# Optimization experiments

Measured on AMD Instinct MI355X. Metric: run time of the kernel, lower is better.

Reference implementation:

```python
import jax, jax.numpy as jnp
import numpy as np

B, G, P, H = 32, 5000, 5000, 64
N = B * G
E_CO, E_GG = 1600000, 100000

def _bn(x, g, b):
    # BatchNorm1d in training mode: biased batch stats, eps=1e-5
    m = x.mean(0); v = x.var(0)
    return g * (x - m) * jax.lax.rsqrt(v + 1e-5) + b

def _renorm(t):
    # nn.Embedding(max_norm=True) -> rows renormed to L2 norm <= 1
    n = jnp.linalg.norm(t, axis=1, keepdims=True)
    return t * jnp.minimum(1.0, 1.0 / jnp.maximum(n, 1e-12))

def _sgconv(x, src, dst, w, W, b):
    # SGConv(K=1): gcn_norm (self-loops w=1, symmetric deg norm) spmm, then Linear
    n = x.shape[0]
    sl = jnp.arange(n)
    s = jnp.concatenate([src, sl]); d = jnp.concatenate([dst, sl])
    ww = jnp.concatenate([w, jnp.ones((n,), x.dtype)])
    deg = jax.ops.segment_sum(ww, d, num_segments=n)
    dinv = jnp.where(deg > 0, jax.lax.rsqrt(deg), 0.0)
    coef = dinv[s] * ww * dinv[d]
    agg = jax.ops.segment_sum(coef[:, None] * x[s], d, num_segments=n)
    return agg @ W.T + b

def _mlp3(x, W, b, g, bt):
    # MLP([h,h,h]): Lin-BN-ReLU-Lin-BN (trailing ReLU stripped by [:-1])
    h = jax.nn.relu(_bn(x @ W[0].T + b[0], g[0], bt[0]))
    return _bn(h @ W[1].T + b[1], g[1], bt[1])

def _gears(x, pert_idx, ei_co, w_co, ei_go, w_go, ei_bg, w_bg,
           gene_tab, pos_tab, go_tab, bg_tab, bn_g, bn_b, sg_W, sg_b,
           mlp_W, mlp_b, mlp_g, mlp_bt,
           rec_W1, rec_b1, rec_g1, rec_bt1, rec_W2, rec_b2, rec_g2, rec_bt2,
           indv_w1, indv_b1,
           cg_W1, cg_b1, cg_g1, cg_bt1, cg_W2, cg_b2, cg_g2, cg_bt2,
           indv_w2, indv_b2):
    nb = pert_idx.shape[0]
    ng = gene_tab.shape[0]
    emb = jnp.tile(_renorm(gene_tab), (nb, 1))                     # [B*G,H]
    base = jax.nn.relu(_bn(emb, bn_g[0], bn_b[0]))                 # bn_emb + emb_trans
    pos = jnp.tile(_renorm(pos_tab), (nb, 1))
    pos = _sgconv(pos, ei_co[0], ei_co[1], w_co, sg_W[0], sg_b[0]) # 1 gene-pos GNN layer, no trailing relu
    base = base + 0.2 * pos
    base = _mlp3(base, mlp_W[1], mlp_b[1], mlp_g[1], mlp_bt[1])    # emb_trans_v2
    pgo = _sgconv(_renorm(go_tab), ei_go[0], ei_go[1], w_go, sg_W[1], sg_b[1])
    pbg = _sgconv(_renorm(bg_tab), ei_bg[0], ei_bg[1], w_bg, sg_W[2], sg_b[2])
    pglob = _mlp3(pgo + pbg, mlp_W[0], mlp_b[0], mlp_g[0], mlp_bt[0])  # pert_emb_comb_trans
    base = base.reshape(nb, ng, -1)
    # one valid pert per graph -> pert_track reduces to a gather; pert_fuse then broadcast-add
    emb_total = _mlp3(pglob[pert_idx], mlp_W[2], mlp_b[2], mlp_g[2], mlp_bt[2])  # [B,H]
    base = base + emb_total[:, None, :]
    base = base.reshape(nb * ng, -1)
    base = jax.nn.relu(_bn(base, bn_g[1], bn_b[1]))                # bn_pert_base + transform
    h = jax.nn.relu(_bn(base @ rec_W1.T + rec_b1, rec_g1, rec_bt1))
    out = _bn(h @ rec_W2.T + rec_b2, rec_g2, rec_bt2).reshape(nb, ng, -1)
    w1 = jnp.einsum('bgh,gh->bg', out, indv_w1) + indv_b1          # per-gene decoder 1
    cg = jax.nn.relu(_bn(w1 @ cg_W1.T + cg_b1, cg_g1, cg_bt1))
    cg = _bn(cg @ cg_W2.T + cg_b2, cg_g2, cg_bt2)                  # cross_gene_state [B,H]
    cat = jnp.concatenate([w1[..., None], jnp.broadcast_to(cg[:, None, :], (nb, ng, cg.shape[-1]))], -1)
    out2 = jnp.einsum('bgk,gk->bg', cat, indv_w2) + indv_b2        # per-gene decoder 2
    return out2 + x.reshape(nb, ng)

def setup_inputs():
    ks = jax.random.split(jax.random.key(0), 48)
    rn = lambda i, sh, s=0.05: jax.random.normal(ks[i], sh, jnp.float32) * s
    return {
        "x": rn(0, (N,), 1.0),
        "pert_idx": jax.random.randint(ks[1], (B,), 0, P),
        "ei_co": jax.random.randint(ks[2], (2, E_CO), 0, N),
        "w_co": jax.random.uniform(ks[3], (E_CO,), jnp.float32),
        "ei_go": jax.random.randint(ks[4], (2, E_GG), 0, P),
        "w_go": jax.random.uniform(ks[5], (E_GG,), jnp.float32),
        "ei_bg": jax.random.randint(ks[6], (2, E_GG), 0, P),
        "w_bg": jax.random.uniform(ks[7], (E_GG,), jnp.float32),
        "gene_tab": rn(8, (G, H), 1.0),
        "pos_tab": rn(9, (G, H), 1.0),
        "go_tab": rn(10, (P, H), 1.0),
        "bg_tab": rn(11, (P, H), 1.0),
        "bn_g": jnp.ones((2, H)), "bn_b": jnp.zeros((2, H)),
        "sg_W": rn(12, (3, H, H)), "sg_b": jnp.zeros((3, H)),
        "mlp_W": rn(13, (3, 2, H, H)), "mlp_b": jnp.zeros((3, 2, H)),
        "mlp_g": jnp.ones((3, 2, H)), "mlp_bt": jnp.zeros((3, 2, H)),
        "rec_W1": rn(14, (2 * H, H)), "rec_b1": jnp.zeros((2 * H,)),
        "rec_g1": jnp.ones((2 * H,)), "rec_bt1": jnp.zeros((2 * H,)),
        "rec_W2": rn(15, (H, 2 * H)), "rec_b2": jnp.zeros((H,)),
        "rec_g2": jnp.ones((H,)), "rec_bt2": jnp.zeros((H,)),
        "indv_w1": rn(16, (G, H)), "indv_b1": rn(17, (G,)),
        "cg_W1": rn(18, (H, G), 0.01), "cg_b1": jnp.zeros((H,)),
        "cg_g1": jnp.ones((H,)), "cg_bt1": jnp.zeros((H,)),
        "cg_W2": rn(19, (H, H)), "cg_b2": jnp.zeros((H,)),
        "cg_g2": jnp.ones((H,)), "cg_bt2": jnp.zeros((H,)),
        "indv_w2": rn(20, (G, H + 1)), "indv_b2": rn(21, (G,)),
    }

def reference(x, pert_idx, ei_co, w_co, ei_go, w_go, ei_bg, w_bg,
              gene_tab, pos_tab, go_tab, bg_tab, bn_g, bn_b, sg_W, sg_b,
              mlp_W, mlp_b, mlp_g, mlp_bt,
              rec_W1, rec_b1, rec_g1, rec_bt1, rec_W2, rec_b2, rec_g2, rec_bt2,
              indv_w1, indv_b1,
              cg_W1, cg_b1, cg_g1, cg_bt1, cg_W2, cg_b2, cg_g2, cg_bt2,
              indv_w2, indv_b2):
    return _gears(x, pert_idx, ei_co, w_co, ei_go, w_go, ei_bg, w_bg,
                  gene_tab, pos_tab, go_tab, bg_tab, bn_g, bn_b, sg_W, sg_b,
                  mlp_W, mlp_b, mlp_g, mlp_bt,
                  rec_W1, rec_b1, rec_g1, rec_bt1, rec_W2, rec_b2, rec_g2, rec_bt2,
                  indv_w1, indv_b1,
                  cg_W1, cg_b1, cg_g1, cg_bt1, cg_W2, cg_b2, cg_g2, cg_bt2,
                  indv_w2, indv_b2)
```

## Files before the change

kernel.cpp:

```cpp
#include <hip/hip_runtime.h>

typedef unsigned int u32;
typedef unsigned short u16;

constexpr int Gn  = 5000;
constexpr int Bn  = 32;
constexpr int Pn  = 5000;
constexpr int Nn  = Bn * Gn;
constexpr int ECO = 1600000;
constexpr int EGG = 100000;
constexpr int NTILES = Nn / 128;
constexpr int PTILES = 40;

constexpr int oS1 = 0, oS2 = 128, oS3 = 256, oS4 = 384, oS5 = 640, oSG = 768, oSP1 = 896, oSP2 = 1024;
constexpr int oZERO = 1536;
constexpr int oA1 = 2048, oB1 = 2112, oA2 = 2176, oB2 = 2240;
constexpr int oA4 = 2304, oB4 = 2432;
constexpr int oA5 = 2560, oB5 = 2624;
constexpr int oAG = 2688, oBG = 2752;
constexpr int oAP1 = 2816, oBP1 = 2880, oAP2 = 2944, oBP2 = 3008;
constexpr int oAvec = 3072, oCvec = 3136, oCcP = 3200;
constexpr int oM  = 4096, oM1 = 8192;
constexpr int oE2 = 16384, oEMB = 18432, oCGRAW = 20480, oCG2 = 22528;
constexpr int oRG  = 24576;
constexpr int oRP  = oRG  + Gn * 64;
constexpr int oQ   = oRP  + Gn * 64;
constexpr int oRGO = oQ   + Gn * 64;
constexpr int oRBG = oRGO + Pn * 64;
constexpr int oAGO = oRBG + Pn * 64;
constexpr int oABG = oAGO + Pn * 64;
constexpr int oM1B = oABG + Pn * 64;
constexpr int oM2B = oM1B + Pn * 64;
constexpr int oDGO = oM2B + Pn * 64;
constexpr int oDBG = oDGO + Pn;
constexpr int oDEG = oDBG + Pn;
constexpr int oW1  = oDEG + Nn;
constexpr int oBUF0 = oW1 + Nn;
constexpr int oBUF1 = oBUF0 + Nn * 64;
constexpr size_t WS_FLOATS = (size_t)oBUF1 + (size_t)Nn * 64;

__device__ inline u16 f2bf(float f) {
  u32 u = __float_as_uint(f);
  u = (u + 0x7fffu + ((u >> 16) & 1u)) >> 16;
  return (u16)u;
}
__device__ inline float bflo(u32 v) { return __uint_as_float(v << 16); }
__device__ inline float bfhi(u32 v) { return __uint_as_float(v & 0xffff0000u); }
__device__ inline float bf2f(u16 v) { return __uint_as_float((u32)v << 16); }

typedef __attribute__((ext_vector_type(8))) short short8v;
typedef __attribute__((ext_vector_type(4))) float f32x4;

__global__ __launch_bounds__(256) void kzero(float* p, int n) {
  int i = blockIdx.x * 256 + threadIdx.x;
  if (i < n) p[i] = 0.f;
}

__global__ __launch_bounds__(256) void krenorm(const float* __restrict__ in, float* __restrict__ out,
                                               float* __restrict__ stats, u16* __restrict__ outb, int rows) {
  int lane = threadIdx.x & 63, wv = threadIdx.x >> 6;
  int gw = blockIdx.x * 4 + wv, nw = gridDim.x * 4;
  float ps = 0.f, pq = 0.f;
  for (int r = gw; r < rows; r += nw) {
    float v = in[r * 64 + lane];
    float sq = v * v;
    for (int off = 32; off; off >>= 1) sq += __shfl_xor(sq, off, 64);
    float nn = sqrtf(sq);
    float s = fminf(1.f, 1.f / fmaxf(nn, 1e-12f));
    float o = v * s;
    out[r * 64 + lane] = o;
    if (outb) outb[r * 64 + lane] = f2bf(o);
    ps += o; pq += o * o;
  }
  if (!stats) return;
  __shared__ float red[4][64], red2[4][64];
  red[wv][lane] = ps; red2[wv][lane] = pq;
  __syncthreads();
  if (wv == 0) {
    float s = red[0][lane] + red[1][lane] + red[2][lane] + red[3][lane];
    float q = red2[0][lane] + red2[1][lane] + red2[2][lane] + red2[3][lane];
    atomicAdd(&stats[lane], s);
    atomicAdd(&stats[64 + lane], q);
  }
}

__global__ void kfin(const float* __restrict__ stats, const float* __restrict__ g,
                     const float* __restrict__ bt, float* __restrict__ a, float* __restrict__ b,
                     int cols, float invn) {
  int c = blockIdx.x * 64 + threadIdx.x;
  if (c >= cols) return;
  float mean = stats[c] * invn;
  float var = stats[cols + c] * invn - mean * mean;
  float sc = g[c] * rsqrtf(var + 1e-5f);
  a[c] = sc;
  b[c] = bt[c] - mean * sc;
}

__global__ __launch_bounds__(256) void ksmallmat(const float* __restrict__ A, const float* __restrict__ Bm,
                                                 float alpha, const float* __restrict__ bias,
                                                 const float* __restrict__ bv1, const float* __restrict__ bv2,
                                                 float beta, float* __restrict__ Mout, int mpitch,
                                                 float* __restrict__ cvec) {
  __shared__ float As[4096], Bs[4096];
  int t = threadIdx.x;
  for (int m = 0; m < 16; m++) { As[m * 256 + t] = A[m * 256 + t]; Bs[m * 256 + t] = Bm[m * 256 + t]; }
  __syncthreads();
  int j = t & 63, ig = t >> 6;
  for (int ii = 0; ii < 16; ii++) {
    int i = ig * 16 + ii;
    float acc = 0.f;
    for (int k = 0; k < 64; k++) acc += As[i * 64 + k] * Bs[k * 64 + j];
    Mout[i * mpitch + j] = alpha * acc;
  }
  if (cvec && t < 64) {
    float acc = bias ? bias[t] : 0.f;
    for (int k = 0; k < 64; k++) {
      float bb = (bv1 ? bv1[k] : 0.f) + (bv2 ? bv2[k] : 0.f);
      acc += beta * As[t * 64 + k] * bb;
    }
    cvec[t] = acc;
  }
}

__global__ __launch_bounds__(256) void khist(const int* __restrict__ dst, int* __restrict__ cnt,
                                             int* __restrict__ ticket, int E) {
  int e = blockIdx.x * 256 + threadIdx.x;
  if (e < E) ticket[e] = atomicAdd(&cnt[dst[e]], 1);
}

__global__ __launch_bounds__(256) void kscan1(const int* __restrict__ cnt, int* __restrict__ bsum, int n) {
  __shared__ int sh[256];
  int b = blockIdx.x, t = threadIdx.x;
  int base = b * 1024 + t * 4;
  int s = 0;
#pragma unroll
  for (int j = 0; j < 4; j++) { int i = base + j; if (i < n) s += cnt[i]; }
  sh[t] = s; __syncthreads();
  for (int d = 128; d; d >>= 1) { if (t < d) sh[t] += sh[t + d]; __syncthreads(); }
  if (t == 0) bsum[b] = sh[0];
}
__global__ __launch_bounds__(256) void kscan2(int* bsum, int nb, int* off_n) {
  __shared__ int sh[256];
  int t = threadIdx.x;
  int v = (t < nb) ? bsum[t] : 0;
  sh[t] = v;
  __syncthreads();
  for (int d = 1; d < 256; d <<= 1) {
    int u = (t >= d) ? sh[t - d] : 0;
    __syncthreads();
    sh[t] += u;
    __syncthreads();
  }
  if (t < nb) bsum[t] = sh[t] - v;
  if (t == nb - 1 && off_n) *off_n = sh[t];
}
__global__ __launch_bounds__(256) void kscan3(int* __restrict__ cnt, const int* __restrict__ bsum, int n) {
  __shared__ int sh[256];
  int b = blockIdx.x, t = threadIdx.x;
  int base = b * 1024 + t * 4;
  int c0 = (base + 0 < n) ? cnt[base + 0] : 0;
  int c1 = (base + 1 < n) ? cnt[base + 1] : 0;
  int c2 = (base + 2 < n) ? cnt[base + 2] : 0;
  int c3 = (base + 3 < n) ? cnt[base + 3] : 0;
  int tot = c0 + c1 + c2 + c3;
  sh[t] = tot; __syncthreads();
  for (int d = 1; d < 256; d <<= 1) {
    int v = (t >= d) ? sh[t - d] : 0;
    __syncthreads();
    sh[t] += v;
    __syncthreads();
  }
  int excl = sh[t] - tot + bsum[b];
  if (base + 0 < n) cnt[base + 0] = excl;
  if (base + 1 < n) cnt[base + 1] = excl + c0;
  if (base + 2 < n) cnt[base + 2] = excl + c0 + c1;
  if (base + 3 < n) cnt[base + 3] = excl + c0 + c1 + c2;
}

__global__ __launch_bounds__(256) void kfillt(const int* __restrict__ src, const int* __restrict__ dst,
                                              const float* __restrict__ w, const int* __restrict__ off,
                                              const int* __restrict__ ticket, float2* __restrict__ pack, int E) {
  int e = blockIdx.x * 256 + threadIdx.x;
  if (e >= E) return;
  int d = dst[e];
  int pos = off[d] + ticket[e];
  pack[pos] = make_float2(w[e], __int_as_float(src[e]));
}

__global__ __launch_bounds__(256) void kdinvrow(const int* __restrict__ off, const float2* __restrict__ pack,
                                                float* __restrict__ dinv, int n) {
  int i = blockIdx.x * 256 + threadIdx.x;
  if (i >= n) return;
  int b0 = off[i], b1 = off[i + 1];
  float s = 1.f;
  for (int j = b0; j < b1; j++) s += pack[j].x;
  dinv[i] = rsqrtf(s);
}

__global__ __launch_bounds__(256) void kgather(const int* __restrict__ off, const float2* __restrict__ pack,
                                               const float* __restrict__ dinv, const float* __restrict__ tab,
                                               u16* __restrict__ aggb, int pitch, int coff, int n) {
  int lane = threadIdx.x & 63;
  int wv = blockIdx.x * 4 + (threadIdx.x >> 6);
  int nw = gridDim.x * 4;
  for (int i = wv; i < n; i += nw) {
    int b0 = off[i], b1 = off[i + 1];
    float di = dinv[i];
    float acc = di * tab[(i % Gn) * 64 + lane];
    for (int base = b0; base < b1; base += 64) {
      int m = b1 - base; if (m > 64) m = 64;
      float cj = 0.f; int idxj = 0;
      if (lane < m) {
        float2 p = pack[base + lane];
        int s = __float_as_int(p.y);
        cj = p.x * dinv[s];
        idxj = (s % Gn) * 64;
      }
      int j = 0;
      for (; j + 1 < m; j += 2) {
        float c0 = __shfl(cj, j, 64);     int i0 = __shfl(idxj, j, 64);
        float c1 = __shfl(cj, j + 1, 64); int i1 = __shfl(idxj, j + 1, 64);
        float t0 = tab[i0 + lane];
        float t1 = tab[i1 + lane];
        acc = fmaf(c0, t0, acc);
        acc = fmaf(c1, t1, acc);
      }
      if (j < m) {
        float c0 = __shfl(cj, j, 64); int i0 = __shfl(idxj, j, 64);
        acc = fmaf(c0, tab[i0 + lane], acc);
      }
    }
    acc *= di;
    aggb[(size_t)i * pitch + coff + lane] = f2bf(acc);
  }
}

template <int K, int OUTC, bool PRE, bool EB, bool PERG, bool STATS, bool OUTF32, bool STATB>
__global__ __launch_bounds__(256, 3) void mfgemm(
    const u16* __restrict__ Xb, const float* __restrict__ Wg, const float* __restrict__ bias,
    const float* __restrict__ pa, const float* __restrict__ pb,
    const float* __restrict__ perg, u16* __restrict__ Ybf, float* __restrict__ stats,
    float* __restrict__ statB, int rows) {
  constexpr int NT  = OUTC / 16;
  constexpr int KH  = K / 32;
  constexpr int SLK = K / 8;
  constexpr int SLO = OUTC / 8;
  constexpr int XROW = (K > OUTC ? K : OUTC) * 2;
  __shared__ __align__(16) unsigned char xsb[128 * XROW];
  __shared__ __align__(16) unsigned char wsb[OUTC * K * 2];
  __shared__ float sstat[STATS ? 2 * OUTC : 1];
  __shared__ float sstatB[STATB ? 128 : 1];
  int t = threadIdx.x;
  int l = t & 63, w = t >> 6, lrow = l & 15, lk = l >> 4;
  int R0 = blockIdx.x * 128;

  for (int idx = t; idx < OUTC * SLK; idx += 256) {
    int oc = idx / SLK, s8 = idx % SLK;
    const float* wp = &Wg[oc * K + s8 * 8];
    uint4 o;
    o.x = (u32)f2bf(wp[0]) | ((u32)f2bf(wp[1]) << 16);
    o.y = (u32)f2bf(wp[2]) | ((u32)f2bf(wp[3]) << 16);
    o.z = (u32)f2bf(wp[4]) | ((u32)f2bf(wp[5]) << 16);
    o.w = (u32)f2bf(wp[6]) | ((u32)f2bf(wp[7]) << 16);
    *(uint4*)&wsb[oc * (2 * K) + ((s8 * 16) ^ ((oc & 7) << 4))] = o;
  }
  if constexpr (STATS) for (int idx = t; idx < 2 * OUTC; idx += 256) sstat[idx] = 0.f;
  if constexpr (STATB) for (int idx = t; idx < 128; idx += 256) sstatB[idx] = 0.f;

#pragma unroll
  for (int m = 0; m < SLK / 2; m++) {
    int f = m * 256 + t;
    int r = f / SLK, s8 = f % SLK;
    uint4 u = *(const uint4*)&Xb[(size_t)(R0 + r) * K + s8 * 8];
    if constexpr (PRE) {
      int c0 = s8 * 8;
      float4 A0 = *(const float4*)&pa[c0];
      float4 A1 = *(const float4*)&pa[c0 + 4];
      const float* pbb = EB ? &pb[((R0 + r) / Gn) * 64] : pb;
      float4 B0 = *(const float4*)&pbb[c0];
      float4 B1 = *(const float4*)&pbb[c0 + 4];
      float v0 = fmaxf(fmaf(A0.x, bflo(u.x), B0.x), 0.f);
      float v1 = fmaxf(fmaf(A0.y, bfhi(u.x), B0.y), 0.f);
      float v2 = fmaxf(fmaf(A0.z, bflo(u.y), B0.z), 0.f);
      float v3 = fmaxf(fmaf(A0.w, bfhi(u.y), B0.w), 0.f);
      float v4 = fmaxf(fmaf(A1.x, bflo(u.z), B1.x), 0.f);
      float v5 = fmaxf(fmaf(A1.y, bfhi(u.z), B1.y), 0.f);
      float v6 = fmaxf(fmaf(A1.z, bflo(u.w), B1.z), 0.f);
      float v7 = fmaxf(fmaf(A1.w, bfhi(u.w), B1.w), 0.f);
      u.x = (u32)f2bf(v0) | ((u32)f2bf(v1) << 16);
      u.y = (u32)f2bf(v2) | ((u32)f2bf(v3) << 16);
      u.z = (u32)f2bf(v4) | ((u32)f2bf(v5) << 16);
      u.w = (u32)f2bf(v6) | ((u32)f2bf(v7) << 16);
    }
    *(uint4*)&xsb[r * XROW + ((s8 * 16) ^ ((r & 7) << 4))] = u;
  }
  float bcol[NT];
#pragma unroll
  for (int nt = 0; nt < NT; nt++) bcol[nt] = bias[nt * 16 + lrow];
  __syncthreads();

  short8v af[2][KH];
#pragma unroll
  for (int rt = 0; rt < 2; rt++)
#pragma unroll
    for (int h = 0; h < KH; h++) {
      int row = w * 32 + rt * 16 + lrow;
      af[rt][h] = *(const short8v*)&xsb[row * XROW + ((h * 64 + lk * 16) ^ ((row & 7) << 4))];
    }
  f32x4 acc[2][NT];
#pragma unroll
  for (int rt = 0; rt < 2; rt++)
#pragma unroll
    for (int nt = 0; nt < NT; nt++) {
      f32x4 z = {0.f, 0.f, 0.f, 0.f};
      acc[rt][nt] = z;
    }
#pragma unroll
  for (int nt = 0; nt < NT; nt++) {
    int brow = nt * 16 + lrow;
#pragma unroll
    for (int h = 0; h < KH; h++) {
      short8v bfr = *(const short8v*)&wsb[brow * (2 * K) + ((h * 64 + lk * 16) ^ ((brow & 7) << 4))];
      acc[0][nt] = __builtin_amdgcn_mfma_f32_16x16x32_bf16(af[0][h], bfr, acc[0][nt], 0, 0, 0);
      acc[1][nt] = __builtin_amdgcn_mfma_f32_16x16x32_bf16(af[1][h], bfr, acc[1][nt], 0, 0, 0);
    }
  }
  __syncthreads();

  float sS[NT], sQ[NT], sB0[NT], sB1[NT];
#pragma unroll
  for (int nt = 0; nt < NT; nt++) { sS[nt] = 0.f; sQ[nt] = 0.f; sB0[nt] = 0.f; sB1[nt] = 0.f; }
  int hiStart = STATB ? (R0 / Gn + 1) * Gn : 0x7fffffff;
  float* Yf = (float*)Ybf;
#pragma unroll
  for (int rt = 0; rt < 2; rt++) {
#pragma unroll
    for (int r = 0; r < 4; r++) {
      int orow = w * 32 + rt * 16 + lk * 4 + r;
      int grow = R0 + orow;
      bool valid = grow < rows;
      int qoff = 0;
      if constexpr (PERG) qoff = (grow % Gn) * 64;
#pragma unroll
      for (int nt = 0; nt < NT; nt++) {
        float v = acc[rt][nt][r] + bcol[nt];
        if constexpr (PERG) v += perg[qoff + nt * 16 + lrow];
        if (valid) {
          if constexpr (STATS) { sS[nt] += v; sQ[nt] += v * v; }
          if constexpr (STATB) { if (grow >= hiStart) sB1[nt] += v; else sB0[nt] += v; }
        }
        if constexpr (OUTF32) {
          if (valid) Yf[(size_t)grow * OUTC + nt * 16 + lrow] = v;
        } else {
          *(u16*)&xsb[orow * (2 * OUTC) + ((2 * (nt * 16 + lrow)) ^ ((orow & 7) << 4))] = f2bf(v);
        }
      }
    }
  }
  if constexpr (STATS) {
#pragma unroll
    for (int nt = 0; nt < NT; nt++) {
      atomicAdd(&sstat[nt * 16 + lrow], sS[nt]);
      atomicAdd(&sstat[OUTC + nt * 16 + lrow], sQ[nt]);
    }
  }
  if constexpr (STATB) {
#pragma unroll
    for (int nt = 0; nt < NT; nt++) {
      atomicAdd(&sstatB[nt * 16 + lrow], sB0[nt]);
      atomicAdd(&sstatB[64 + nt * 16 + lrow], sB1[nt]);
    }
  }
  __syncthreads();

  if constexpr (!OUTF32) {
#pragma unroll
    for (int m = 0; m < SLO / 2; m++) {
      int f = m * 256 + t;
      int r = f / SLO, c8 = f % SLO;
      uint4 o = *(const uint4*)&xsb[r * (2 * OUTC) + ((16 * c8) ^ ((r & 7) << 4))];
      *(uint4*)&Ybf[(size_t)(R0 + r) * OUTC + c8 * 8] = o;
    }
  }
  if constexpr (STATS)
    for (int idx = t; idx < 2 * OUTC; idx += 256) atomicAdd(&stats[idx], sstat[idx]);
  if constexpr (STATB) {
    int bLo = R0 / Gn;
    for (int idx = t; idx < 128; idx += 256) {
      int b = bLo + (idx >> 6);
      if (b < Bn) atomicAdd(&statB[b * 64 + (idx & 63)], sstatB[idx]);
    }
  }
}

__global__ __launch_bounds__(256) void kfinS3e2(const float* __restrict__ S2, const float* __restrict__ g,
                                                const float* __restrict__ bt, const float* __restrict__ a2,
                                                const float* __restrict__ b2, const float* __restrict__ emb,
                                                const float* __restrict__ S3B,
                                                float* __restrict__ Avec, float* __restrict__ e2) {
  __shared__ float a3s[64], b3s[64];
  int t = threadIdx.x;
  if (t < 64) {
    float a2c = a2[t], b2c = b2[t];
    float su = 0.f, sxc = 0.f, sc2 = 0.f;
    for (int b = 0; b < Bn; b++) {
      float cb = b2c + emb[b * 64 + t];
      float sb = S3B[b * 64 + t];
      su += cb;
      sxc += cb * sb;
      sc2 += cb * cb;
    }
    float Su = a2c * S2[t] + (float)Gn * su;
    float Sq = a2c * a2c * S2[64 + t] + 2.f * a2c * sxc + (float)Gn * sc2;
    float mean = Su * (1.f / Nn);
    float var = Sq * (1.f / Nn) - mean * mean;
    float sc = g[t] * rsqrtf(var + 1e-5f);
    float sh = bt[t] - mean * sc;
    a3s[t] = sc; b3s[t] = sh;
    Avec[t] = sc * a2c;
  }
  __syncthreads();
  for (int idx = t; idx < 2048; idx += 256) {
    int c = idx & 63;
    e2[idx] = a3s[c] * (b2[c] + emb[idx]) + b3s[c];
  }
}

__global__ __launch_bounds__(256) void k13_kernel(const u16* __restrict__ R2, const float* __restrict__ a5,
                                                  const float* __restrict__ b5, const float* __restrict__ iw1,
                                                  const float* __restrict__ ib1, float* __restrict__ w1out,
                                                  int rows) {
  int t = blockIdx.x * 256 + threadIdx.x;
  int i = t >> 4, j = t & 15;
  if (i >= rows) return;
  int g = i % Gn;
  uint2 u = *(const uint2*)&R2[(size_t)i * 64 + j * 4];
  float rx = bflo(u.x), ry = bfhi(u.x), rz = bflo(u.y), rw = bfhi(u.y);
  float4 a = ((const float4*)a5)[j];
  float4 b = ((const float4*)b5)[j];
  float4 w = ((const float4*)iw1)[g * 16 + j];
  float p = (a.x * rx + b.x) * w.x + (a.y * ry + b.y) * w.y +
            (a.z * rz + b.z) * w.z + (a.w * rw + b.w) * w.w;
  for (int off = 8; off; off >>= 1) p += __shfl_xor(p, off, 64);
  if (j == 0) w1out[i] = p + ib1[g];
}

__global__ __launch_bounds__(256) void kinitcg(const float* __restrict__ cgb1, float* __restrict__ cgraw) {
  int idx = blockIdx.x * 256 + threadIdx.x;
  if (idx < Bn * 64) cgraw[idx] = cgb1[idx & 63];
}

__global__ __launch_bounds__(256) void kcg1s(const float* __restrict__ w1, const float* __restrict__ cgW1,
                                             float* __restrict__ cgraw) {
  __shared__ float w1s[64 * 36];
  __shared__ float cgs[64 * 65];
  int t = threadIdx.x;
  int k0 = blockIdx.x * 64;
  int kmax = Gn - k0; if (kmax > 64) kmax = 64;
  for (int idx = t; idx < 2048; idx += 256) {
    int row = idx >> 6, k = idx & 63;
    w1s[k * 36 + row] = (k < kmax) ? w1[row * Gn + k0 + k] : 0.f;
  }
  for (int idx = t; idx < 4096; idx += 256) {
    int col = idx >> 6, k = idx & 63;
    cgs[k * 65 + col] = (k < kmax) ? cgW1[col * Gn + k0 + k] : 0.f;
  }
  __syncthreads();
  int col = t & 63, rg = t >> 6;
  float acc[8];
#pragma unroll
  for (int i = 0; i < 8; i++) acc[i] = 0.f;
  for (int k = 0; k < 64; k++) {
    float wk = cgs[k * 65 + col];
    const float* wr = &w1s[k * 36 + rg * 8];
    float4 r0 = *(const float4*)wr;
    float4 r1 = *(const float4*)(wr + 4);
    acc[0] = fmaf(r0.x, wk, acc[0]);
    acc[1] = fmaf(r0.y, wk, acc[1]);
    acc[2] = fmaf(r0.z, wk, acc[2]);
    acc[3] = fmaf(r0.w, wk, acc[3]);
    acc[4] = fmaf(r1.x, wk, acc[4]);
    acc[5] = fmaf(r1.y, wk, acc[5]);
    acc[6] = fmaf(r1.z, wk, acc[6]);
    acc[7] = fmaf(r1.w, wk, acc[7]);
  }
#pragma unroll
  for (int i = 0; i < 8; i++) atomicAdd(&cgraw[(rg * 8 + i) * 64 + col], acc[i]);
}

__global__ __launch_bounds__(256) void kcg2(const float* __restrict__ cgraw, const float* __restrict__ g1,
                                            const float* __restrict__ bt1, const float* __restrict__ W2,
                                            const float* __restrict__ b2, const float* __restrict__ g2,
                                            const float* __restrict__ bt2, float* __restrict__ cg2out) {
  int t = threadIdx.x, c = t & 63, bg = t >> 6;
  __shared__ float hmid[2048], sred[4][64], qred[4][64], asc[64], bsh[64];
  float y[8];
  float ps = 0.f, pq = 0.f;
  for (int jb = 0; jb < 8; jb++) {
    int b = bg * 8 + jb;
    float v = cgraw[b * 64 + c];
    y[jb] = v; ps += v; pq += v * v;
  }
  sred[bg][c] = ps; qred[bg][c] = pq;
  __syncthreads();
  if (t < 64) {
    float s = sred[0][t] + sred[1][t] + sred[2][t] + sred[3][t];
    float q = qred[0][t] + qred[1][t] + qred[2][t] + qred[3][t];
    float mean = s * (1.f / 32.f), var = q * (1.f / 32.f) - mean * mean;
    float sc = g1[t] * rsqrtf(var + 1e-5f);
    asc[t] = sc; bsh[t] = bt1[t] - mean * sc;
  }
  __syncthreads();
  for (int jb = 0; jb < 8; jb++) { int b = bg * 8 + jb; hmid[b * 64 + c] = fmaxf(asc[c] * y[jb] + bsh[c], 0.f); }
  __syncthreads();
  ps = 0.f; pq = 0.f;
  for (int jb = 0; jb < 8; jb++) {
    int b = bg * 8 + jb;
    float a = b2[c];
    for (int k = 0; k < 64; k++) a += hmid[b * 64 + k] * W2[c * 64 + k];
    y[jb] = a; ps += a; pq += a * a;
  }
  sred[bg][c] = ps; qred[bg][c] = pq;
  __syncthreads();
  if (t < 64) {
    float s = sred[0][t] + sred[1][t] + sred[2][t] + sred[3][t];
    float q = qred[0][t] + qred[1][t] + qred[2][t] + qred[3][t];
    float mean = s * (1.f / 32.f), var = q * (1.f / 32.f) - mean * mean;
    float sc = g2[t] * rsqrtf(var + 1e-5f);
    asc[t] = sc; bsh[t] = bt2[t] - mean * sc;
  }
  __syncthreads();
  for (int jb = 0; jb < 8; jb++) { int b = bg * 8 + jb; cg2out[b * 64 + c] = asc[c] * y[jb] + bsh[c]; }
}

__global__ __launch_bounds__(256) void kemb(const u16* __restrict__ m2, const float* __restrict__ aP2,
                                            const float* __restrict__ bP2, const int* __restrict__ pidx,
                                            const float* __restrict__ Wm, const float* __restrict__ bv,
                                            const float* __restrict__ gg, const float* __restrict__ btv,
                                            float* __restrict__ emb) {
  int t = threadIdx.x, c = t & 63, bg = t >> 6;
  __shared__ float xin[2048], hmid[2048], sred[4][64], qred[4][64], asc[64], bsh[64];
  for (int idx = t; idx < 2048; idx += 256) {
    int b = idx >> 6, cc = idx & 63;
    xin[idx] = aP2[cc] * bf2f(m2[(size_t)pidx[b] * 64 + cc]) + bP2[cc];
  }
  __syncthreads();
  float y[8];
  float ps = 0.f, pq = 0.f;
  for (int jb = 0; jb < 8; jb++) {
    int b = bg * 8 + jb;
    float a = bv[c];
    for (int k = 0; k < 64; k++) a += xin[b * 64 + k] * Wm[c * 64 + k];
    y[jb] = a; ps += a; pq += a * a;
  }
  sred[bg][c] = ps; qred[bg][c] = pq;
  __syncthreads();
  if (t < 64) {
    float s = sred[0][t] + sred[1][t] + sred[2][t] + sred[3][t];
    float q = qred[0][t] + qred[1][t] + qred[2][t] + qred[3][t];
    float mean = s * (1.f / 32.f), var = q * (1.f / 32.f) - mean * mean;
    float sc = gg[t] * rsqrtf(var + 1e-5f);
    asc[t] = sc; bsh[t] = btv[t] - mean * sc;
  }
  __syncthreads();
  for (int jb = 0; jb < 8; jb++) { int b = bg * 8 + jb; hmid[b * 64 + c] = fmaxf(asc[c] * y[jb] + bsh[c], 0.f); }
  __syncthreads();
  ps = 0.f; pq = 0.f;
  for (int jb = 0; jb < 8; jb++) {
    int b = bg * 8 + jb;
    float a = bv[64 + c];
    for (int k = 0; k < 64; k++) a += hmid[b * 64 + k] * Wm[4096 + c * 64 + k];
    y[jb] = a; ps += a; pq += a * a;
  }
  sred[bg][c] = ps; qred[bg][c] = pq;
  __syncthreads();
  if (t < 64) {
    float s = sred[0][t] + sred[1][t] + sred[2][t] + sred[3][t];
    float q = qred[0][t] + qred[1][t] + qred[2][t] + qred[3][t];
    float mean = s * (1.f / 32.f), var = q * (1.f / 32.f) - mean * mean;
    float sc = gg[64 + t] * rsqrtf(var + 1e-5f);
    asc[t] = sc; bsh[t] = btv[64 + t] - mean * sc;
  }
  __syncthreads();
  for (int jb = 0; jb < 8; jb++) { int b = bg * 8 + jb; emb[b * 64 + c] = asc[c] * y[jb] + bsh[c]; }
}

__global__ __launch_bounds__(256) void kfinal(const float* __restrict__ w1, const float* __restrict__ cg2,
                                              const float* __restrict__ iw2, const float* __restrict__ ib2,
                                              const float* __restrict__ x, float* __restrict__ out) {
  __shared__ float iws[64 * 65], cgs[2048];
  int t = threadIdx.x;
  int g0 = blockIdx.x * 64;
  for (int idx = t; idx < 64 * 65; idx += 256) {
    int gi = g0 * 65 + idx;
    iws[idx] = (gi < Gn * 65) ? iw2[gi] : 0.f;
  }
  for (int idx = t; idx < 2048; idx += 256) cgs[idx] = cg2[idx];
  __syncthreads();
  int gl = t & 63, bg = t >> 6;
  int g = g0 + gl;
  if (g >= Gn) return;
  float bias = ib2[g];
  for (int jb = 0; jb < 8; jb++) {
    int b = bg * 8 + jb;
    float acc = w1[b * Gn + g] * iws[gl * 65] + bias;
    for (int k = 0; k < 64; k++) acc += cgs[b * 64 + k] * iws[gl * 65 + 1 + k];
    out[b * Gn + g] = acc + x[b * Gn + g];
  }
}

extern "C" void kernel_launch(void* const* d_in, const int* in_sizes, int n_in,
                              void* d_out, int out_size, void* d_ws, size_t ws_size,
                              hipStream_t stream) {
  (void)in_sizes; (void)n_in; (void)out_size;
  if (ws_size < WS_FLOATS * sizeof(float)) return;

  const float* x        = (const float*)d_in[0];
  const int*   pert_idx = (const int*)d_in[1];
  const int*   ei_co    = (const int*)d_in[2];
  const float* w_co     = (const float*)d_in[3];
  const int*   ei_go    = (const int*)d_in[4];
  const float* w_go     = (const float*)d_in[5];
  const int*   ei_bg    = (const int*)d_in[6];
  const float* w_bg     = (const float*)d_in[7];
  const float* gene_tab = (const float*)d_in[8];
  const float* pos_tab  = (const float*)d_in[9];
  const float* go_tab   = (const float*)d_in[10];
  const float* bg_tab   = (const float*)d_in[11];
  const float* bn_g     = (const float*)d_in[12];
  const float* bn_b     = (const float*)d_in[13];
  const float* sg_W     = (const float*)d_in[14];
  const float* sg_b     = (const float*)d_in[15];
  const float* mlp_W    = (const float*)d_in[16];
  const float* mlp_b    = (const float*)d_in[17];
  const float* mlp_g    = (const float*)d_in[18];
  const float* mlp_bt   = (const float*)d_in[19];
  const float* rec_W1   = (const float*)d_in[20];
  const float* rec_b1   = (const float*)d_in[21];
  const float* rec_g1   = (const float*)d_in[22];
  const float* rec_bt1  = (const float*)d_in[23];
  const float* rec_W2   = (const float*)d_in[24];
  const float* rec_b2   = (const float*)d_in[25];
  const float* rec_g2   = (const float*)d_in[26];
  const float* rec_bt2  = (const float*)d_in[27];
  const float* indv_w1  = (const float*)d_in[28];
  const float* indv_b1  = (const float*)d_in[29];
  const float* cg_W1    = (const float*)d_in[30];
  const float* cg_b1    = (const float*)d_in[31];
  const float* cg_g1    = (const float*)d_in[32];
  const float* cg_bt1   = (const float*)d_in[33];
  const float* cg_W2    = (const float*)d_in[34];
  const float* cg_b2    = (const float*)d_in[35];
  const float* cg_g2    = (const float*)d_in[36];
  const float* cg_bt2   = (const float*)d_in[37];
  const float* indv_w2  = (const float*)d_in[38];
  const float* indv_b2  = (const float*)d_in[39];

  float* W = (float*)d_ws;
  float* buf0 = W + oBUF0;
  float* buf1 = W + oBUF1;

  int*    co_cnt    = (int*)(buf1);
  int*    sbsum     = (int*)(buf1 + 320128);
  float2* co_pack   = (float2*)(buf1 + 400000);
  int*    go_cnt    = (int*)(buf1 + 3700000);
  float2* go_pack   = (float2*)(buf1 + 3720000);
  int*    bg_cnt    = (int*)(buf1 + 4000000);
  float2* bg_pack   = (float2*)(buf1 + 4020000);
  int*    co_ticket = (int*)(buf1 + 4500000);
  int*    go_ticket = (int*)(buf1 + 6200000);
  int*    bg_ticket = (int*)(buf1 + 6400000);
  u16*    pgi       = (u16*)(buf1 + 6600000);
  u16*    RGB       = (u16*)(buf1 + 6800000);

  kzero<<<8, 256, 0, stream>>>(W, 2048);
  kzero<<<8, 256, 0, stream>>>(W + oE2, 2048);
  kzero<<<15, 256, 0, stream>>>(buf1 + 6800000 + 160000, 3840);
  kzero<<<30, 256, 0, stream>>>(buf1 + 6600000 + 320000, 7680);
  krenorm<<<160, 256, 0, stream>>>(gene_tab, W + oRG, W + oSG, RGB, Gn);
  krenorm<<<160, 256, 0, stream>>>(pos_tab, W + oRP, nullptr, nullptr, Gn);
  krenorm<<<160, 256, 0, stream>>>(go_tab, W + oRGO, nullptr, nullptr, Pn);
  krenorm<<<160, 256, 0, stream>>>(bg_tab, W + oRBG, nullptr, nullptr, Pn);
  kfin<<<1, 64, 0, stream>>>(W + oSG, bn_g, bn_b, W + oAG, W + oBG, 64, 1.f / Gn);
  ksmallmat<<<1, 256, 0, stream>>>(mlp_W + 8192, sg_W, 0.2f, mlp_b + 128, sg_b, nullptr, 0.2f,
                                   W + oM, 64, W + oCvec);
  ksmallmat<<<1, 256, 0, stream>>>(mlp_W, sg_W + 4096, 1.f, nullptr, nullptr, nullptr, 0.f,
                                   W + oM1, 128, nullptr);
  ksmallmat<<<1, 256, 0, stream>>>(mlp_W, sg_W + 8192, 1.f, mlp_b, sg_b + 64, sg_b + 128, 1.f,
                                   W + oM1 + 64, 128, W + oCcP);
  mfgemm<64, 64, true, false, false, false, true, false><<<PTILES, 256, 0, stream>>>(
      RGB, mlp_W + 8192, W + oCvec, W + oAG, W + oBG, nullptr, (u16*)(W + oQ), nullptr, nullptr, Gn);

  kzero<<<(5001 + 255) / 256, 256, 0, stream>>>((float*)go_cnt, 5001);
  khist<<<(EGG + 255) / 256, 256, 0, stream>>>(ei_go + EGG, go_cnt, go_ticket, EGG);
  kscan1<<<5, 256, 0, stream>>>(go_cnt, sbsum, Pn);
  kscan2<<<1, 256, 0, stream>>>(sbsum, 5, go_cnt + Pn);
  kscan3<<<5, 256, 0, stream>>>(go_cnt, sbsum, Pn);
  kfillt<<<(EGG + 255) / 256, 256, 0, stream>>>(ei_go, ei_go + EGG, w_go, go_cnt, go_ticket, go_pack, EGG);
  kdinvrow<<<(Pn + 255) / 256, 256, 0, stream>>>(go_cnt, go_pack, W + oDGO, Pn);
  kgather<<<512, 256, 0, stream>>>(go_cnt, go_pack, W + oDGO, W + oRGO, pgi, 128, 0, Pn);

  kzero<<<(5001 + 255) / 256, 256, 0, stream>>>((float*)bg_cnt, 5001);
  khist<<<(EGG + 255) / 256, 256, 0, stream>>>(ei_bg + EGG, bg_cnt, bg_ticket, EGG);
  kscan1<<<5, 256, 0, stream>>>(bg_cnt, sbsum, Pn);
  kscan2<<<1, 256, 0, stream>>>(sbsum, 5, bg_cnt + Pn);
  kscan3<<<5, 256, 0, stream>>>(bg_cnt, sbsum, Pn);
  kfillt<<<(EGG + 255) / 256, 256, 0, stream>>>(ei_bg, ei_bg + EGG, w_bg, bg_cnt, bg_ticket, bg_pack, EGG);
  kdinvrow<<<(Pn + 255) / 256, 256, 0, stream>>>(bg_cnt, bg_pack, W + oDBG, Pn);
  kgather<<<512, 256, 0, stream>>>(bg_cnt, bg_pack, W + oDBG, W + oRBG, pgi, 128, 64, Pn);

  mfgemm<128, 64, false, false, false, true, false, false><<<PTILES, 256, 0, stream>>>(
      pgi, W + oM1, W + oCcP, nullptr, nullptr, nullptr, (u16*)(W + oM1B), W + oSP1, nullptr, Pn);
  kfin<<<1, 64, 0, stream>>>(W + oSP1, mlp_g, mlp_bt, W + oAP1, W + oBP1, 64, 1.f / Pn);
  mfgemm<64, 64, true, false, false, true, false, false><<<PTILES, 256, 0, stream>>>(
      (u16*)(W + oM1B), mlp_W + 4096, mlp_b + 64, W + oAP1, W + oBP1, nullptr,
      (u16*)(W + oM2B), W + oSP2, nullptr, Pn);
  kfin<<<1, 64, 0, stream>>>(W + oSP2, mlp_g + 64, mlp_bt + 64, W + oAP2, W + oBP2, 64, 1.f / Pn);
  kemb<<<1, 256, 0, stream>>>((u16*)(W + oM2B), W + oAP2, W + oBP2, pert_idx,
                              mlp_W + 16384, mlp_b + 256, mlp_g + 256, mlp_bt + 256, W + oEMB);

  kzero<<<(160001 + 255) / 256, 256, 0, stream>>>((float*)co_cnt, 160001);
  khist<<<(ECO + 255) / 256, 256, 0, stream>>>(ei_co + ECO, co_cnt, co_ticket, ECO);
  kscan1<<<157, 256, 0, stream>>>(co_cnt, sbsum, Nn);
  kscan2<<<1, 256, 0, stream>>>(sbsum, 157, co_cnt + Nn);
  kscan3<<<157, 256, 0, stream>>>(co_cnt, sbsum, Nn);
  kfillt<<<(ECO + 255) / 256, 256, 0, stream>>>(ei_co, ei_co + ECO, w_co, co_cnt, co_ticket, co_pack, ECO);
  kdinvrow<<<(Nn + 255) / 256, 256, 0, stream>>>(co_cnt, co_pack, W + oDEG, Nn);
  kgather<<<2048, 256, 0, stream>>>(co_cnt, co_pack, W + oDEG, W + oRP, (u16*)buf0, 64, 0, Nn);

  mfgemm<64, 64, false, false, true, true, false, false><<<NTILES, 256, 0, stream>>>(
      (const u16*)buf0, W + oM, W + oZERO, nullptr, nullptr, W + oQ, (u16*)buf1, W + oS1, nullptr, Nn);
  kfin<<<1, 64, 0, stream>>>(W + oS1, mlp_g + 128, mlp_bt + 128, W + oA1, W + oB1, 64, 1.f / Nn);
  mfgemm<64, 64, true, false, false, true, false, true><<<NTILES, 256, 0, stream>>>(
      (const u16*)buf1, mlp_W + 12288, mlp_b + 192, W + oA1, W + oB1, nullptr,
      (u16*)buf0, W + oS2, W + oE2, Nn);
  kfin<<<1, 64, 0, stream>>>(W + oS2, mlp_g + 192, mlp_bt + 192, W + oA2, W + oB2, 64, 1.f / Nn);
  kfinS3e2<<<1, 256, 0, stream>>>(W + oS2, bn_g + 64, bn_b + 64, W + oA2, W + oB2, W + oEMB,
                                  W + oE2, W + oAvec, W + oE2);
  mfgemm<64, 128, true, true, false, true, false, false><<<NTILES, 256, 0, stream>>>(
      (const u16*)buf0, rec_W1, rec_b1, W + oAvec, W + oE2, nullptr, (u16*)buf1, W + oS4, nullptr, Nn);
  kfin<<<2, 64, 0, stream>>>(W + oS4, rec_g1, rec_bt1, W + oA4, W + oB4, 128, 1.f / Nn);
  mfgemm<128, 64, true, false, false, true, false, false><<<NTILES, 256, 0, stream>>>(
      (const u16*)buf1, rec_W2, rec_b2, W + oA4, W + oB4, nullptr, (u16*)buf0, W + oS5, nullptr, Nn);
  kfin<<<1, 64, 0, stream>>>(W + oS5, rec_g2, rec_bt2, W + oA5, W + oB5, 64, 1.f / Nn);
  k13_kernel<<<(Nn * 16 + 255) / 256, 256, 0, stream>>>((const u16*)buf0, W + oA5, W + oB5, indv_w1, indv_b1,
                                                        W + oW1, Nn);
  kinitcg<<<8, 256, 0, stream>>>(cg_b1, W + oCGRAW);
  kcg1s<<<(Gn + 63) / 64, 256, 0, stream>>>(W + oW1, cg_W1, W + oCGRAW);
  kcg2<<<1, 256, 0, stream>>>(W + oCGRAW, cg_g1, cg_bt1, cg_W2, cg_b2, cg_g2, cg_bt2, W + oCG2);
  kfinal<<<(Gn + 63) / 64, 256, 0, stream>>>(W + oW1, W + oCG2, indv_w2, indv_b2, x, (float*)d_out);
}
```

Measured before the change: 724.6 us.

## Build co-expression CSR with two-level bucketed partition instead of global histogram

Replaces the global per-node histogram, three-pass scan, ticketed fill and separate degree pass for the 1.6M-edge graph with a two-level counting sort. Edges are first bucketed by dst>>8 into 625 buckets using shared-memory atomics, then each bucket builds its local CSR offsets, degree normalisation and packed edges in shared memory. This aims to cut global atomic contention and the number of launches and passes over the edge arrays. It adds an intermediate staging buffer and relies on Nn being exactly 625*256.

```diff
diff --git a/kernel.cpp b/kernel.cpp
--- a/kernel.cpp
+++ b/kernel.cpp
@@ -11,6 +11,7 @@
 constexpr int EGG = 100000;
 constexpr int NTILES = Nn / 128;
 constexpr int PTILES = 40;
+constexpr int NBK = 625;
 
 constexpr int oS1 = 0, oS2 = 128, oS3 = 256, oS4 = 384, oS5 = 640, oSG = 768, oSP1 = 896, oSP2 = 1024;
 constexpr int oZERO = 1536;
@@ -195,6 +196,103 @@
   float s = 1.f;
   for (int j = b0; j < b1; j++) s += pack[j].x;
   dinv[i] = rsqrtf(s);
+}
+
+__global__ __launch_bounds__(256) void kpcnt(const int* __restrict__ dst, int* __restrict__ bcnt, int E) {
+  __shared__ int h[NBK];
+  int t = threadIdx.x;
+  for (int i = t; i < NBK; i += 256) h[i] = 0;
+  __syncthreads();
+  int stride = gridDim.x * 256;
+  for (int e = blockIdx.x * 256 + t; e < E; e += stride) atomicAdd(&h[dst[e] >> 8], 1);
+  __syncthreads();
+  for (int i = t; i < NBK; i += 256) { int c = h[i]; if (c) atomicAdd(&bcnt[i], c); }
+}
+__global__ __launch_bounds__(256) void kpscan(const int* __restrict__ bcnt, int* __restrict__ bbase,
+                                              int* __restrict__ bcur, int* __restrict__ offN) {
+  __shared__ int sh[256];
+  int t = threadIdx.x;
+  int i0 = t * 3;
+  int c[3];
+  int s = 0;
+#pragma unroll
+  for (int j = 0; j < 3; j++) { int i = i0 + j; c[j] = (i < NBK) ? bcnt[i] : 0; s += c[j]; }
+  sh[t] = s;
+  __syncthreads();
+  for (int d = 1; d < 256; d <<= 1) {
+    int u = (t >= d) ? sh[t - d] : 0;
+    __syncthreads();
+    sh[t] += u;
+    __syncthreads();
+  }
+  int base = sh[t] - s;
+#pragma unroll
+  for (int j = 0; j < 3; j++) {
+    int i = i0 + j;
+    if (i < NBK) { bbase[i] = base; bcur[i] = base; }
+    base += c[j];
+  }
+  if (t == 255) { bbase[NBK] = base; *offN = base; }
+}
+__global__ __launch_bounds__(256) void kpscat(const int* __restrict__ src, const int* __restrict__ dst,
+                                              const float* __restrict__ w, int* __restrict__ bcur,
+                                              float2* __restrict__ sa, u16* __restrict__ sb, int E) {
+  __shared__ int h[NBK];
+  int t = threadIdx.x;
+  constexpr int EPB = (ECO + 255) / 256;
+  int e0 = blockIdx.x * EPB;
+  int e1 = e0 + EPB; if (e1 > E) e1 = E;
+  for (int i = t; i < NBK; i += 256) h[i] = 0;
+  __syncthreads();
+  for (int e = e0 + t; e < e1; e += 256) atomicAdd(&h[dst[e] >> 8], 1);
+  __syncthreads();
+  for (int i = t; i < NBK; i += 256) {
+    int c = h[i];
+    h[i] = c ? atomicAdd(&bcur[i], c) : 0;
+  }
+  __syncthreads();
+  for (int e = e0 + t; e < e1; e += 256) {
+    int d = dst[e];
+    int pos = atomicAdd(&h[d >> 8], 1);
+    sa[pos] = make_float2(w[e], __int_as_float(src[e]));
+    sb[pos] = (u16)(d & 255);
+  }
+}
+__global__ __launch_bounds__(256) void kpcsr(const int* __restrict__ bbase, const float2* __restrict__ sa,
+                                             const u16* __restrict__ sb, int* __restrict__ off,
+                                             float2* __restrict__ pack, float* __restrict__ dinv) {
+  __shared__ int rh[256];
+  __shared__ int sc[256];
+  __shared__ float ws[256];
+  int bk = blockIdx.x, t = threadIdx.x;
+  int s0 = bbase[bk], s1 = bbase[bk + 1];
+  rh[t] = 0; ws[t] = 0.f;
+  __syncthreads();
+  for (int i = s0 + t; i < s1; i += 256) {
+    int r = sb[i];
+    atomicAdd(&rh[r], 1);
+    atomicAdd(&ws[r], sa[i].x);
+  }
+  __syncthreads();
+  int cnt = rh[t];
+  sc[t] = cnt;
+  __syncthreads();
+  for (int d = 1; d < 256; d <<= 1) {
+    int u = (t >= d) ? sc[t - d] : 0;
+    __syncthreads();
+    sc[t] += u;
+    __syncthreads();
+  }
+  int gpos = s0 + sc[t] - cnt;
+  int grow = (bk << 8) + t;
+  off[grow] = gpos;
+  dinv[grow] = rsqrtf(1.f + ws[t]);
+  rh[t] = gpos;
+  __syncthreads();
+  for (int i = s0 + t; i < s1; i += 256) {
+    int pos = atomicAdd(&rh[sb[i]], 1);
+    pack[pos] = sa[i];
+  }
 }
 
 __global__ __launch_bounds__(256) void kgather(const int* __restrict__ off, const float2* __restrict__ pack,
@@ -660,18 +758,22 @@
   float* buf0 = W + oBUF0;
   float* buf1 = W + oBUF1;
 
-  int*    co_cnt    = (int*)(buf1);
+  int*    co_off    = (int*)(buf1);
+  int*    bbase     = (int*)(buf1 + 200000);
+  int*    bcur      = (int*)(buf1 + 201000);
+  int*    bcnt      = (int*)(buf1 + 202000);
   int*    sbsum     = (int*)(buf1 + 320128);
   float2* co_pack   = (float2*)(buf1 + 400000);
   int*    go_cnt    = (int*)(buf1 + 3700000);
   float2* go_pack   = (float2*)(buf1 + 3720000);
   int*    bg_cnt    = (int*)(buf1 + 4000000);
   float2* bg_pack   = (float2*)(buf1 + 4020000);
-  int*    co_ticket = (int*)(buf1 + 4500000);
+  u16*    co_sb     = (u16*)(buf1 + 4500000);
   int*    go_ticket = (int*)(buf1 + 6200000);
   int*    bg_ticket = (int*)(buf1 + 6400000);
   u16*    pgi       = (u16*)(buf1 + 6600000);
   u16*    RGB       = (u16*)(buf1 + 6800000);
+  float2* co_sa     = (float2*)(buf1 + 6963840);
 
   kzero<<<8, 256, 0, stream>>>(W, 2048);
   kzero<<<8, 256, 0, stream>>>(W + oE2, 2048);
@@ -719,14 +821,12 @@
   kemb<<<1, 256, 0, stream>>>((u16*)(W + oM2B), W + oAP2, W + oBP2, pert_idx,
                               mlp_W + 16384, mlp_b + 256, mlp_g + 256, mlp_bt + 256, W + oEMB);
 
-  kzero<<<(160001 + 255) / 256, 256, 0, stream>>>((float*)co_cnt, 160001);
-  khist<<<(ECO + 255) / 256, 256, 0, stream>>>(ei_co + ECO, co_cnt, co_ticket, ECO);
-  kscan1<<<157, 256, 0, stream>>>(co_cnt, sbsum, Nn);
-  kscan2<<<1, 256, 0, stream>>>(sbsum, 157, co_cnt + Nn);
-  kscan3<<<157, 256, 0, stream>>>(co_cnt, sbsum, Nn);
-  kfillt<<<(ECO + 255) / 256, 256, 0, stream>>>(ei_co, ei_co + ECO, w_co, co_cnt, co_ticket, co_pack, ECO);
-  kdinvrow<<<(Nn + 255) / 256, 256, 0, stream>>>(co_cnt, co_pack, W + oDEG, Nn);
-  kgather<<<2048, 256, 0, stream>>>(co_cnt, co_pack, W + oDEG, W + oRP, (u16*)buf0, 64, 0, Nn);
+  kzero<<<3, 256, 0, stream>>>((float*)bcnt, NBK);
+  kpcnt<<<256, 256, 0, stream>>>(ei_co + ECO, bcnt, ECO);
+  kpscan<<<1, 256, 0, stream>>>(bcnt, bbase, bcur, co_off + Nn);
+  kpscat<<<256, 256, 0, stream>>>(ei_co, ei_co + ECO, w_co, bcur, co_sa, co_sb, ECO);
+  kpcsr<<<NBK, 256, 0, stream>>>(bbase, co_sa, co_sb, co_off, co_pack, W + oDEG);
+  kgather<<<2048, 256, 0, stream>>>(co_off, co_pack, W + oDEG, W + oRP, (u16*)buf0, 64, 0, Nn);
 
   mfgemm<64, 64, false, false, true, true, false, false><<<NTILES, 256, 0, stream>>>(
       (const u16*)buf0, W + oM, W + oZERO, nullptr, nullptr, W + oQ, (u16*)buf1, W + oS1, nullptr, Nn);
```

Measured after the change: 694.6 us. 4.1% less time.
